# Kernel optimization log

Measured on AMD Instinct MI355X. Metric: run time of the kernel, lower is better.

Reference implementation:

```python
import jax, jax.numpy as jnp
import numpy as np

B, S, D_MODEL = 2, 2048, 2048
D_STATE, D_CONV, EXPAND = 16, 4, 2
D_INNER = EXPAND * D_MODEL  # 4096


def setup_inputs() -> dict:
    key = jax.random.key(0)
    ks = jax.random.split(key, 7)
    nrm = lambda k, shape, sc: jax.random.normal(k, shape, jnp.float32) * sc
    x = nrm(ks[0], (B, S, D_MODEL), 1.0)
    W_in = nrm(ks[1], (2 * D_INNER, D_MODEL), 0.02)          # in_proj (no bias)
    conv_w = nrm(ks[2], (D_INNER, 1, D_CONV), 0.1)            # depthwise conv1d
    conv_b = nrm(ks[3], (D_INNER,), 0.02)
    W_dt = nrm(ks[4], (D_INNER, D_INNER), 0.001)              # dt_proj weight
    b_dt = jnp.full((D_INNER,), -8.0, jnp.float32)            # keeps softplus(dt) tiny -> stable scan
    A_log = jnp.log(jnp.arange(1, D_STATE + 1, dtype=jnp.float32))[None, :]  # [1, d_state]
    W_out = nrm(ks[5], (D_MODEL, D_INNER), 1e-4)              # out_proj (no bias)
    return dict(x=x, W_in=W_in, conv_w=conv_w, conv_b=conv_b,
                W_dt=W_dt, b_dt=b_dt, A_log=A_log, W_out=W_out)


def reference(x, W_in, conv_w, conv_b, W_dt, b_dt, A_log, W_out):
    # in_proj then split into ssm branch and gate
    xz = jnp.einsum('bsd,ed->bse', x, W_in)            # [B,S,2*D_INNER]
    xi, gate = jnp.split(xz, 2, axis=-1)
    # depthwise causal conv (torch pads d_conv-1 both sides then truncates to S == left-pad only)
    xc = jnp.transpose(xi, (0, 2, 1))                  # [B,D_INNER,S]
    xc = jax.lax.conv_general_dilated(
        xc, conv_w, window_strides=(1,), padding=[(D_CONV - 1, 0)],
        dimension_numbers=('NCH', 'OIH', 'NCH'), feature_group_count=D_INNER)
    xc = xc + conv_b[None, :, None]
    xs = jax.nn.silu(jnp.transpose(xc, (0, 2, 1)))     # [B,S,D_INNER]
    # selective scan (only first d_state channels of x and dt are used)
    A = -jnp.exp(A_log[0])                             # [D_STATE]
    dt = jax.nn.softplus(jnp.einsum('bsd,ed->bse', xs, W_dt[:D_STATE]) + b_dt[:D_STATE])  # [B,S,D_STATE]
    u = xs[:, :, :D_STATE]                             # [B,S,D_STATE]

    def step(h, inp):
        x_t, dt_t = inp
        h = h * (1.0 + dt_t) + x_t
        return h, (h * A).sum(-1)                      # y_t: [B]

    h0 = jnp.zeros((B, D_STATE), xs.dtype)
    _, ys = jax.lax.scan(step, h0, (jnp.swapaxes(u, 0, 1), jnp.swapaxes(dt, 0, 1)))
    result = jnp.swapaxes(ys, 0, 1)                    # [B,S]
    # original: expand to d_inner, sum (== *d_inner), broadcast back over d_inner
    ssm_out = jnp.broadcast_to((result * D_INNER)[..., None], (B, S, D_INNER))
    y = ssm_out * jax.nn.sigmoid(gate)
    return jnp.einsum('bse,de->bsd', y, W_out)         # [B,S,D_MODEL]
```

## Files before the change

kernel.cpp:

```cpp
#include <hip/hip_runtime.h>
#include <hip/hip_bf16.h>
#include <math.h>

using bf16_t = __bf16;
using bf16x8 = __attribute__((ext_vector_type(8))) __bf16;
using f32x4  = __attribute__((ext_vector_type(4))) float;

typedef __attribute__((address_space(1))) const void* gas_ptr;
typedef __attribute__((address_space(3))) void*       las_ptr;

#define BATCH    2
#define SEQ      2048
#define DMODEL   2048
#define DINNER   4096
#define DSTATE   16
#define NROWS    (BATCH * SEQ)

#define CAST_C0  (2 * DINNER * DMODEL / 8)
#define CAST_C1  (NROWS * DMODEL / 8)
#define CAST_C2  (DMODEL * DINNER / 8)
#define CAST_BLOCKS ((CAST_C0 + CAST_C1 + CAST_C2) / 256)

__global__ __launch_bounds__(256)
void cast_all_kernel(const float* __restrict__ s0, bf16_t* __restrict__ d0,
                     const float* __restrict__ s1, bf16_t* __restrict__ d1,
                     const float* __restrict__ s2, bf16_t* __restrict__ d2)
{
    int i = blockIdx.x * 256 + threadIdx.x;
    const float* src; bf16_t* dst; int j;
    if (i < CAST_C0)                  { src = s0; dst = d0; j = i; }
    else if (i < CAST_C0 + CAST_C1)   { src = s1; dst = d1; j = i - CAST_C0; }
    else                              { src = s2; dst = d2; j = i - CAST_C0 - CAST_C1; }
    size_t off = (size_t)j * 8;
    float4 a = *(const float4*)(src + off);
    float4 b = *(const float4*)(src + off + 4);
    bf16x8 o;
    o[0] = (bf16_t)a.x; o[1] = (bf16_t)a.y; o[2] = (bf16_t)a.z; o[3] = (bf16_t)a.w;
    o[4] = (bf16_t)b.x; o[5] = (bf16_t)b.y; o[6] = (bf16_t)b.z; o[7] = (bf16_t)b.w;
    *(bf16x8*)(dst + off) = o;
}

#define GBAR()     asm volatile("s_barrier" ::: "memory")
#define WLGKM0()   asm volatile("s_waitcnt lgkmcnt(0)" ::: "memory")
#define WVM0()     asm volatile("s_waitcnt vmcnt(0)" ::: "memory")

#define MM(m, n, av, bv) \
    acc[m][n] = __builtin_amdgcn_mfma_f32_16x16x32_bf16(av, bv, acc[m][n], 0, 0, 0)

#define MFMA_COL2(nA, nB, bA, bB)                                   \
    MM(0, nA, a0, bA); MM(0, nB, a0, bB); MM(1, nA, a1, bA); MM(1, nB, a1, bB); \
    MM(2, nA, a2, bA); MM(2, nB, a2, bB); MM(3, nA, a3, bA); MM(3, nB, a3, bB); \
    MM(4, nA, a4, bA); MM(4, nB, a4, bB); MM(5, nA, a5, bA); MM(5, nB, a5, bB); \
    MM(6, nA, a6, bA); MM(6, nB, a6, bB); MM(7, nA, a7, bA); MM(7, nB, a7, bB)

__global__ __launch_bounds__(512, 2)
void gemm1_256(const bf16_t* __restrict__ A, const bf16_t* __restrict__ B,
               float* __restrict__ outf, bf16_t* __restrict__ outg)
{
    constexpr int K  = DMODEL;
    constexpr int NT = K / 64;

    __shared__ bf16_t As[2][256 * 64];
    __shared__ bf16_t Bs[2][256 * 64];

    const int t    = threadIdx.x;
    const int w    = t >> 6;
    const int lane = t & 63;
    const int wm   = w >> 2;
    const int wn   = w & 3;
    const int lo   = lane & 15;
    const int q    = lane >> 4;
    const int swz  = lo & 7;

    const int m0 = blockIdx.y * 256;
    const int n0 = blockIdx.x * 256;

    const int r_l   = lane >> 3;
    const int cb    = (lane & 7) ^ r_l;
    const int laneg = r_l * K + cb * 8;

    const bf16_t* Abase = A + (size_t)(m0 + w * 32) * K;
    const bf16_t* Bbase = B + (size_t)(n0 + w * 32) * K;

#define STAGE_A(BUF, kk) do {                                                  \
    _Pragma("unroll")                                                          \
    for (int c = 0; c < 4; ++c)                                                \
        __builtin_amdgcn_global_load_lds(                                      \
            (gas_ptr)(Abase + (kk) + c * 8 * K + laneg),                       \
            (las_ptr)&As[BUF][(w * 32 + c * 8) * 64], 16, 0, 0);               \
} while (0)
#define STAGE_B(BUF, kk) do {                                                  \
    _Pragma("unroll")                                                          \
    for (int c = 0; c < 4; ++c)                                                \
        __builtin_amdgcn_global_load_lds(                                      \
            (gas_ptr)(Bbase + (kk) + c * 8 * K + laneg),                       \
            (las_ptr)&Bs[BUF][(w * 32 + c * 8) * 64], 16, 0, 0);               \
} while (0)

#define LDA_F(BUF, m, s) \
    (*(const bf16x8*)&As[BUF][(wm * 128 + (m) * 16 + lo) * 64 + ((((s) * 4 + q) ^ swz) * 8)])
#define LDB_F(BUF, n, s) \
    (*(const bf16x8*)&Bs[BUF][(wn * 64  + (n) * 16 + lo) * 64 + ((((s) * 4 + q) ^ swz) * 8)])

    f32x4 acc[8][4];
#pragma unroll
    for (int i = 0; i < 8; ++i)
#pragma unroll
        for (int j = 0; j < 4; ++j) acc[i][j] = (f32x4){0.f, 0.f, 0.f, 0.f};

    STAGE_A(0, 0);
    STAGE_B(0, 0);
    WVM0();
    GBAR();

#define TILE_STEP(CUR, NXT, tkv) do {                                          \
    const int  k1_  = ((tkv) + 1) * 64;                                        \
    const bool pre_ = ((tkv) + 1) < NT;                                        \
    bf16x8 a0, a1, a2, a3, a4, a5, a6, a7, b0, b1, b2, b3;                     \
                   \
    a0 = LDA_F(CUR, 0, 0); a1 = LDA_F(CUR, 1, 0);                              \
    a2 = LDA_F(CUR, 2, 0); a3 = LDA_F(CUR, 3, 0);                              \
    a4 = LDA_F(CUR, 4, 0); a5 = LDA_F(CUR, 5, 0);                              \
    a6 = LDA_F(CUR, 6, 0); a7 = LDA_F(CUR, 7, 0);                              \
    b0 = LDB_F(CUR, 0, 0); b1 = LDB_F(CUR, 1, 0);                              \
    if (pre_) STAGE_A(NXT, k1_);                                               \
    GBAR(); WLGKM0();                                                          \
    __builtin_amdgcn_s_setprio(1);                                             \
    MFMA_COL2(0, 1, b0, b1);                                                   \
    __builtin_amdgcn_s_setprio(0);                                             \
    GBAR();                                                                    \
                                \
    b2 = LDB_F(CUR, 2, 0); b3 = LDB_F(CUR, 3, 0);                              \
    if (pre_) STAGE_B(NXT, k1_);                                               \
    GBAR(); WLGKM0();                                                          \
    __builtin_amdgcn_s_setprio(1);                                             \
    MFMA_COL2(2, 3, b2, b3);                                                   \
    __builtin_amdgcn_s_setprio(0);                                             \
    GBAR();                                                                    \
                                  \
    a0 = LDA_F(CUR, 0, 1); a1 = LDA_F(CUR, 1, 1);                              \
    a2 = LDA_F(CUR, 2, 1); a3 = LDA_F(CUR, 3, 1);                              \
    a4 = LDA_F(CUR, 4, 1); a5 = LDA_F(CUR, 5, 1);                              \
    a6 = LDA_F(CUR, 6, 1); a7 = LDA_F(CUR, 7, 1);                              \
    b0 = LDB_F(CUR, 0, 1); b1 = LDB_F(CUR, 1, 1);                              \
    GBAR(); WLGKM0();                                                          \
    __builtin_amdgcn_s_setprio(1);                                             \
    MFMA_COL2(0, 1, b0, b1);                                                   \
    __builtin_amdgcn_s_setprio(0);                                             \
    GBAR();                                                                    \
           \
    b2 = LDB_F(CUR, 2, 1); b3 = LDB_F(CUR, 3, 1);                              \
    GBAR(); WLGKM0();                                                          \
    __builtin_amdgcn_s_setprio(1);                                             \
    MFMA_COL2(2, 3, b2, b3);                                                   \
    __builtin_amdgcn_s_setprio(0);                                             \
    WVM0();                                                                    \
    GBAR();                                                                    \
} while (0)

#pragma unroll 1
    for (int tk = 0; tk < NT; tk += 2) {
        TILE_STEP(0, 1, tk);
        TILE_STEP(1, 0, tk + 1);
    }

#pragma unroll
    for (int m = 0; m < 8; ++m) {
        const int rbase = m0 + wm * 128 + m * 16 + q * 4;
#pragma unroll
        for (int n = 0; n < 4; ++n) {
            const int col = n0 + wn * 64 + n * 16 + lo;
#pragma unroll
            for (int rr = 0; rr < 4; ++rr) {
                float v   = acc[m][n][rr];
                int   row = rbase + rr;
                if (col < DINNER) {
                    outf[(size_t)row * DINNER + col] = v;
                } else {
                    float sg = 1.f / (1.f + __expf(-v));
                    outg[(size_t)row * DINNER + (col - DINNER)] = (bf16_t)sg;
                }
            }
        }
    }
}

__global__ __launch_bounds__(256)
void gemm_bt2(const bf16_t* __restrict__ A, const bf16_t* __restrict__ B, int K,
              float* __restrict__ outf, const float* __restrict__ rowscale)
{
    constexpr int LDK = 64;
    __shared__ bf16_t As[128 * LDK];
    __shared__ bf16_t Bs[128 * LDK];

    const int t    = threadIdx.x;
    const int m0   = blockIdx.y * 128;
    const int n0   = blockIdx.x * 128;
    const int w    = t >> 6;
    const int lane = t & 63;
    const int wr   = (w >> 1) * 64;
    const int wc   = (w & 1) * 64;
    const int lo   = lane & 15;
    const int q    = lane >> 4;

    const int r_l  = lane >> 3;
    const int cb   = (lane & 7) ^ r_l;
    const int laneA = (w * 32 + r_l) * K + cb * 8;
    const bf16_t* Abase = A + (size_t)m0 * K;
    const bf16_t* Bbase = B + (size_t)n0 * K;

    f32x4 acc[4][4];
#pragma unroll
    for (int i = 0; i < 4; ++i)
#pragma unroll
        for (int j = 0; j < 4; ++j) acc[i][j] = (f32x4){0.f, 0.f, 0.f, 0.f};

    for (int k0 = 0; k0 < K; k0 += 64) {
#pragma unroll
        for (int c = 0; c < 4; ++c) {
            const int uoff   = k0 + c * 8 * K;
            const int lo_off = (w * 32 + c * 8) * LDK;
            __builtin_amdgcn_global_load_lds((gas_ptr)(Abase + uoff + laneA),
                                             (las_ptr)&As[lo_off], 16, 0, 0);
            __builtin_amdgcn_global_load_lds((gas_ptr)(Bbase + uoff + laneA),
                                             (las_ptr)&Bs[lo_off], 16, 0, 0);
        }
        __syncthreads();

        const int swz = lo & 7;
#pragma unroll
        for (int ks = 0; ks < 2; ++ks) {
            const int kk = ((ks * 4 + q) ^ swz) * 8;
            bf16x8 af[4], bfv[4];
#pragma unroll
            for (int mi = 0; mi < 4; ++mi)
                af[mi] = *(const bf16x8*)&As[(wr + mi * 16 + lo) * LDK + kk];
#pragma unroll
            for (int ni = 0; ni < 4; ++ni)
                bfv[ni] = *(const bf16x8*)&Bs[(wc + ni * 16 + lo) * LDK + kk];
#pragma unroll
            for (int mi = 0; mi < 4; ++mi)
#pragma unroll
                for (int ni = 0; ni < 4; ++ni)
                    acc[mi][ni] = __builtin_amdgcn_mfma_f32_16x16x32_bf16(
                        af[mi], bfv[ni], acc[mi][ni], 0, 0, 0);
        }
        __syncthreads();
    }

#pragma unroll
    for (int mi = 0; mi < 4; ++mi) {
#pragma unroll
        for (int ni = 0; ni < 4; ++ni) {
            const int col   = n0 + wc + ni * 16 + lo;
            const int rbase = m0 + wr + mi * 16 + q * 4;
#pragma unroll
            for (int rr = 0; rr < 4; ++rr) {
                int row = rbase + rr;
                outf[(size_t)row * DMODEL + col] =
                    acc[mi][ni][rr] * (4096.0f * rowscale[row]);
            }
        }
    }
}

#define RROWS 4
__global__ __launch_bounds__(256)
void conv_dt_kernel(const float* __restrict__ xi, const float* __restrict__ cw,
                    const float* __restrict__ cbias, const float* __restrict__ wdt,
                    const float* __restrict__ bdt, float* __restrict__ uT,
                    float* __restrict__ dtT)
{
    const int r0 = blockIdx.x * RROWS;
    const int t  = threadIdx.x;
    const int s0 = r0 & (SEQ - 1);
    const int b  = r0 >> 11;

    float xsv[RROWS][16];
#pragma unroll
    for (int j = 0; j < 4; ++j) {
        const int c = t * 4 + j * 1024;
        float4 w0 = *(const float4*)(cw + (c + 0) * 4);
        float4 w1 = *(const float4*)(cw + (c + 1) * 4);
        float4 w2 = *(const float4*)(cw + (c + 2) * 4);
        float4 w3 = *(const float4*)(cw + (c + 3) * 4);
        float4 cbv = *(const float4*)(cbias + c);
        float4 xr[RROWS + 3];
#pragma unroll
        for (int i = 0; i < RROWS + 3; ++i) {
            int ss = s0 - 3 + i;
            if (ss >= 0)
                xr[i] = *(const float4*)(xi + (size_t)(r0 - 3 + i) * DINNER + c);
            else
                xr[i] = make_float4(0.f, 0.f, 0.f, 0.f);
        }
#pragma unroll
        for (int rr = 0; rr < RROWS; ++rr) {
            float4 a = xr[rr], bv = xr[rr + 1], cc = xr[rr + 2], d = xr[rr + 3];
            float v0 = cbv.x + w0.x * a.x + w0.y * bv.x + w0.z * cc.x + w0.w * d.x;
            float v1 = cbv.y + w1.x * a.y + w1.y * bv.y + w1.z * cc.y + w1.w * d.y;
            float v2 = cbv.z + w2.x * a.z + w2.y * bv.z + w2.z * cc.z + w2.w * d.z;
            float v3 = cbv.w + w3.x * a.w + w3.y * bv.w + w3.z * cc.w + w3.w * d.w;
            xsv[rr][j * 4 + 0] = v0 / (1.f + __expf(-v0));
            xsv[rr][j * 4 + 1] = v1 / (1.f + __expf(-v1));
            xsv[rr][j * 4 + 2] = v2 / (1.f + __expf(-v2));
            xsv[rr][j * 4 + 3] = v3 / (1.f + __expf(-v3));
        }
    }

    if (t < 4) {
#pragma unroll
        for (int rr = 0; rr < RROWS; ++rr)
#pragma unroll
            for (int k = 0; k < 4; ++k)
                uT[b * (DSTATE * SEQ) + (t * 4 + k) * SEQ + (s0 + rr)] = xsv[rr][k];
    }

    float acc[DSTATE][RROWS];
#pragma unroll
    for (int e = 0; e < DSTATE; ++e)
#pragma unroll
        for (int rr = 0; rr < RROWS; ++rr) acc[e][rr] = 0.f;

#pragma unroll
    for (int e = 0; e < DSTATE; ++e) {
        const float* wrow = wdt + (size_t)e * DINNER;
#pragma unroll
        for (int j = 0; j < 4; ++j) {
            float4 wv = *(const float4*)(wrow + t * 4 + j * 1024);
#pragma unroll
            for (int rr = 0; rr < RROWS; ++rr)
                acc[e][rr] += wv.x * xsv[rr][j * 4 + 0] + wv.y * xsv[rr][j * 4 + 1]
                            + wv.z * xsv[rr][j * 4 + 2] + wv.w * xsv[rr][j * 4 + 3];
        }
    }

#pragma unroll
    for (int e = 0; e < DSTATE; ++e)
#pragma unroll
        for (int rr = 0; rr < RROWS; ++rr) {
            float v = acc[e][rr];
#pragma unroll
            for (int off = 32; off > 0; off >>= 1) v += __shfl_down(v, off);
            acc[e][rr] = v;
        }
    __shared__ float red[4][DSTATE][RROWS];
    const int w = t >> 6;
    if ((t & 63) == 0) {
#pragma unroll
        for (int e = 0; e < DSTATE; ++e)
#pragma unroll
            for (int rr = 0; rr < RROWS; ++rr) red[w][e][rr] = acc[e][rr];
    }
    __syncthreads();
    if (t < 64) {
        int e = t >> 2, rr = t & 3;
        float tot = red[0][e][rr] + red[1][e][rr] + red[2][e][rr] + red[3][e][rr] + bdt[e];
        float dtv = (tot > 20.f) ? tot : log1pf(__expf(tot));
        dtT[b * (DSTATE * SEQ) + e * SEQ + (s0 + rr)] = dtv;
    }
}

__global__ __launch_bounds__(512)
void scan2_kernel(const float* __restrict__ dtT, const float* __restrict__ uT,
                  const float* __restrict__ A_log, float* __restrict__ result)
{
    __shared__ float cont[SEQ * 17];
    __shared__ float segP[DSTATE][32];
    __shared__ float segH[DSTATE][32];
    __shared__ float hin[DSTATE][32];

    const int b   = blockIdx.x;
    const int t   = threadIdx.x;
    const int n   = t >> 5;
    const int seg = t & 31;
    const float An = -expf(A_log[n]);

    const float* dtp = dtT + b * (DSTATE * SEQ) + n * SEQ + seg * 64;
    const float* up  = uT  + b * (DSTATE * SEQ) + n * SEQ + seg * 64;

    float P = 1.f, H = 0.f;
    for (int i = 0; i < 64; i += 4) {
        float4 dv = *(const float4*)(dtp + i);
        float4 uv = *(const float4*)(up + i);
        float a;
        a = 1.f + dv.x; P *= a; H = H * a + uv.x;
        a = 1.f + dv.y; P *= a; H = H * a + uv.y;
        a = 1.f + dv.z; P *= a; H = H * a + uv.z;
        a = 1.f + dv.w; P *= a; H = H * a + uv.w;
    }
    segP[n][seg] = P;
    segH[n][seg] = H;
    __syncthreads();

    if (t < DSTATE) {
        float h = 0.f;
#pragma unroll
        for (int j = 0; j < 32; ++j) {
            hin[t][j] = h;
            h = segP[t][j] * h + segH[t][j];
        }
    }
    __syncthreads();

    {
        float h = hin[n][seg];
        const int nsw = (n + seg) & 15;
        for (int i = 0; i < 64; i += 4) {
            float4 dv = *(const float4*)(dtp + i);
            float4 uv = *(const float4*)(up + i);
            const int s = seg * 64 + i;
            h = h * (1.f + dv.x) + uv.x; cont[(s + 0) * 17 + nsw] = h * An;
            h = h * (1.f + dv.y) + uv.y; cont[(s + 1) * 17 + nsw] = h * An;
            h = h * (1.f + dv.z) + uv.z; cont[(s + 2) * 17 + nsw] = h * An;
            h = h * (1.f + dv.w) + uv.w; cont[(s + 3) * 17 + nsw] = h * An;
        }
    }
    __syncthreads();

#pragma unroll
    for (int k = 0; k < 4; ++k) {
        const int s = t + k * 512;
        float sum = 0.f;
#pragma unroll
        for (int j = 0; j < DSTATE; ++j) sum += cont[s * 17 + j];
        result[b * SEQ + s] = sum;
    }
}

extern "C" void kernel_launch(void* const* d_in, const int* in_sizes, int n_in,
                              void* d_out, int out_size, void* d_ws, size_t ws_size,
                              hipStream_t stream)
{
    const float* x      = (const float*)d_in[0];
    const float* W_in   = (const float*)d_in[1];
    const float* conv_w = (const float*)d_in[2];
    const float* conv_b = (const float*)d_in[3];
    const float* W_dt   = (const float*)d_in[4];
    const float* b_dt   = (const float*)d_in[5];
    const float* A_log  = (const float*)d_in[6];
    const float* W_out  = (const float*)d_in[7];
    float* out = (float*)d_out;

    const size_t MB = 1u << 20;
    char* w = (char*)d_ws;
    bf16_t* xb   = (bf16_t*)(w);
    bf16_t* wib  = (bf16_t*)(w + 16 * MB);
    bf16_t* wob  = (bf16_t*)(w + 48 * MB);
    float*  xi   = (float*) (w + 64 * MB);
    bf16_t* g    = (bf16_t*)(w + 128 * MB);
    float*  uT   = (float*) (w + 160 * MB);
    float*  dtT  = (float*) (w + 160 * MB + 262144);
    float*  res  = (float*) (w + 160 * MB + 2 * 262144);

    cast_all_kernel<<<CAST_BLOCKS, 256, 0, stream>>>(W_in, wib, x, xb, W_out, wob);

    gemm1_256<<<dim3(32, 16), 512, 0, stream>>>(xb, wib, xi, g);

    conv_dt_kernel<<<NROWS / RROWS, 256, 0, stream>>>(xi, conv_w, conv_b, W_dt, b_dt, uT, dtT);

    scan2_kernel<<<2, 512, 0, stream>>>(dtT, uT, A_log, res);

    gemm_bt2<<<dim3(16, 32), 256, 0, stream>>>(g, wob, DINNER, out, res);
}
```

Before: 510.8 us.

## Split conv/dt kernel and compute dt projection with bf16 MFMA

Splits the fused conv+SiLU+dt-projection kernel in two. The first kernel writes SiLU outputs as bf16 to a workspace buffer. A new MFMA kernel computes the 16-wide dt projection from that buffer, using a bf16 copy of W_dt added to the cast kernel. This replaces the scalar FMA dot products, shuffle reductions and register pressure with matrix instructions. In exchange it adds an extra launch, a roughly 32MB bf16 write and read round trip, and bf16 precision on the dt inputs.

```diff
diff --git a/kernel.cpp b/kernel.cpp
--- a/kernel.cpp
+++ b/kernel.cpp
@@ -3,6 +3,7 @@
 #include <math.h>
 
 using bf16_t = __bf16;
+using bf16x4 = __attribute__((ext_vector_type(4))) __bf16;
 using bf16x8 = __attribute__((ext_vector_type(8))) __bf16;
 using f32x4  = __attribute__((ext_vector_type(4))) float;
 
@@ -19,18 +20,21 @@
 #define CAST_C0  (2 * DINNER * DMODEL / 8)
 #define CAST_C1  (NROWS * DMODEL / 8)
 #define CAST_C2  (DMODEL * DINNER / 8)
-#define CAST_BLOCKS ((CAST_C0 + CAST_C1 + CAST_C2) / 256)
+#define CAST_C3  (DSTATE * DINNER / 8)
+#define CAST_BLOCKS ((CAST_C0 + CAST_C1 + CAST_C2 + CAST_C3) / 256)
 
 __global__ __launch_bounds__(256)
 void cast_all_kernel(const float* __restrict__ s0, bf16_t* __restrict__ d0,
                      const float* __restrict__ s1, bf16_t* __restrict__ d1,
-                     const float* __restrict__ s2, bf16_t* __restrict__ d2)
+                     const float* __restrict__ s2, bf16_t* __restrict__ d2,
+                     const float* __restrict__ s3, bf16_t* __restrict__ d3)
 {
     int i = blockIdx.x * 256 + threadIdx.x;
     const float* src; bf16_t* dst; int j;
-    if (i < CAST_C0)                  { src = s0; dst = d0; j = i; }
-    else if (i < CAST_C0 + CAST_C1)   { src = s1; dst = d1; j = i - CAST_C0; }
-    else                              { src = s2; dst = d2; j = i - CAST_C0 - CAST_C1; }
+    if (i < CAST_C0)                            { src = s0; dst = d0; j = i; }
+    else if (i < CAST_C0 + CAST_C1)             { src = s1; dst = d1; j = i - CAST_C0; }
+    else if (i < CAST_C0 + CAST_C1 + CAST_C2)   { src = s2; dst = d2; j = i - CAST_C0 - CAST_C1; }
+    else                                        { src = s3; dst = d3; j = i - CAST_C0 - CAST_C1 - CAST_C2; }
     size_t off = (size_t)j * 8;
     float4 a = *(const float4*)(src + off);
     float4 b = *(const float4*)(src + off + 4);
@@ -266,17 +270,15 @@
 
 #define RROWS 4
 __global__ __launch_bounds__(256)
-void conv_dt_kernel(const float* __restrict__ xi, const float* __restrict__ cw,
-                    const float* __restrict__ cbias, const float* __restrict__ wdt,
-                    const float* __restrict__ bdt, float* __restrict__ uT,
-                    float* __restrict__ dtT)
+void conv_silu_kernel(const float* __restrict__ xi, const float* __restrict__ cw,
+                      const float* __restrict__ cbias,
+                      bf16_t* __restrict__ xs, float* __restrict__ uT)
 {
     const int r0 = blockIdx.x * RROWS;
     const int t  = threadIdx.x;
     const int s0 = r0 & (SEQ - 1);
     const int b  = r0 >> 11;
 
-    float xsv[RROWS][16];
 #pragma unroll
     for (int j = 0; j < 4; ++j) {
         const int c = t * 4 + j * 1024;
@@ -301,63 +303,58 @@
             float v1 = cbv.y + w1.x * a.y + w1.y * bv.y + w1.z * cc.y + w1.w * d.y;
             float v2 = cbv.z + w2.x * a.z + w2.y * bv.z + w2.z * cc.z + w2.w * d.z;
             float v3 = cbv.w + w3.x * a.w + w3.y * bv.w + w3.z * cc.w + w3.w * d.w;
-            xsv[rr][j * 4 + 0] = v0 / (1.f + __expf(-v0));
-            xsv[rr][j * 4 + 1] = v1 / (1.f + __expf(-v1));
-            xsv[rr][j * 4 + 2] = v2 / (1.f + __expf(-v2));
-            xsv[rr][j * 4 + 3] = v3 / (1.f + __expf(-v3));
-        }
-    }
-
-    if (t < 4) {
-#pragma unroll
-        for (int rr = 0; rr < RROWS; ++rr)
-#pragma unroll
-            for (int k = 0; k < 4; ++k)
-                uT[b * (DSTATE * SEQ) + (t * 4 + k) * SEQ + (s0 + rr)] = xsv[rr][k];
-    }
-
-    float acc[DSTATE][RROWS];
-#pragma unroll
-    for (int e = 0; e < DSTATE; ++e)
-#pragma unroll
-        for (int rr = 0; rr < RROWS; ++rr) acc[e][rr] = 0.f;
-
-#pragma unroll
-    for (int e = 0; e < DSTATE; ++e) {
-        const float* wrow = wdt + (size_t)e * DINNER;
-#pragma unroll
-        for (int j = 0; j < 4; ++j) {
-            float4 wv = *(const float4*)(wrow + t * 4 + j * 1024);
-#pragma unroll
-            for (int rr = 0; rr < RROWS; ++rr)
-                acc[e][rr] += wv.x * xsv[rr][j * 4 + 0] + wv.y * xsv[rr][j * 4 + 1]
-                            + wv.z * xsv[rr][j * 4 + 2] + wv.w * xsv[rr][j * 4 + 3];
-        }
-    }
-
-#pragma unroll
-    for (int e = 0; e < DSTATE; ++e)
-#pragma unroll
-        for (int rr = 0; rr < RROWS; ++rr) {
-            float v = acc[e][rr];
-#pragma unroll
-            for (int off = 32; off > 0; off >>= 1) v += __shfl_down(v, off);
-            acc[e][rr] = v;
-        }
-    __shared__ float red[4][DSTATE][RROWS];
-    const int w = t >> 6;
-    if ((t & 63) == 0) {
-#pragma unroll
-        for (int e = 0; e < DSTATE; ++e)
-#pragma unroll
-            for (int rr = 0; rr < RROWS; ++rr) red[w][e][rr] = acc[e][rr];
-    }
+            float o0 = v0 / (1.f + __expf(-v0));
+            float o1 = v1 / (1.f + __expf(-v1));
+            float o2 = v2 / (1.f + __expf(-v2));
+            float o3 = v3 / (1.f + __expf(-v3));
+            bf16x4 ov;
+            ov[0] = (bf16_t)o0; ov[1] = (bf16_t)o1;
+            ov[2] = (bf16_t)o2; ov[3] = (bf16_t)o3;
+            *(bf16x4*)(xs + (size_t)(r0 + rr) * DINNER + c) = ov;
+            if (j == 0 && t < 4) {
+                uT[b * (DSTATE * SEQ) + (c + 0) * SEQ + (s0 + rr)] = o0;
+                uT[b * (DSTATE * SEQ) + (c + 1) * SEQ + (s0 + rr)] = o1;
+                uT[b * (DSTATE * SEQ) + (c + 2) * SEQ + (s0 + rr)] = o2;
+                uT[b * (DSTATE * SEQ) + (c + 3) * SEQ + (s0 + rr)] = o3;
+            }
+        }
+    }
+}
+
+__global__ __launch_bounds__(256)
+void dt_mfma_kernel(const bf16_t* __restrict__ xs, const bf16_t* __restrict__ wdtb,
+                    const float* __restrict__ bdt, float* __restrict__ dtT)
+{
+    __shared__ float red[4][256];
+    const int t    = threadIdx.x;
+    const int w    = t >> 6;
+    const int lane = t & 63;
+    const int lo   = lane & 15;
+    const int q    = lane >> 4;
+    const int r0   = blockIdx.x * 16;
+
+    const bf16_t* arow = xs   + (size_t)(r0 + lo) * DINNER + w * 1024 + q * 8;
+    const bf16_t* brow = wdtb + (size_t)lo        * DINNER + w * 1024 + q * 8;
+
+    f32x4 acc = (f32x4){0.f, 0.f, 0.f, 0.f};
+#pragma unroll
+    for (int kt = 0; kt < 32; ++kt) {
+        bf16x8 a  = *(const bf16x8*)(arow + kt * 32);
+        bf16x8 bv = *(const bf16x8*)(brow + kt * 32);
+        acc = __builtin_amdgcn_mfma_f32_16x16x32_bf16(a, bv, acc, 0, 0, 0);
+    }
+#pragma unroll
+    for (int i = 0; i < 4; ++i) red[w][lane * 4 + i] = acc[i];
     __syncthreads();
-    if (t < 64) {
-        int e = t >> 2, rr = t & 3;
-        float tot = red[0][e][rr] + red[1][e][rr] + red[2][e][rr] + red[3][e][rr] + bdt[e];
-        float dtv = (tot > 20.f) ? tot : log1pf(__expf(tot));
-        dtT[b * (DSTATE * SEQ) + e * SEQ + (s0 + rr)] = dtv;
+
+    {
+        const int ln  = t >> 2;
+        const int i   = t & 3;
+        const int e   = ln & 15;
+        const int row = r0 + (ln >> 4) * 4 + i;
+        float v = red[0][t] + red[1][t] + red[2][t] + red[3][t] + bdt[e];
+        float dtv = (v > 20.f) ? v : log1pf(__expf(v));
+        dtT[(row >> 11) * (DSTATE * SEQ) + e * SEQ + (row & (SEQ - 1))] = dtv;
     }
 }
 
@@ -452,12 +449,17 @@
     float*  uT   = (float*) (w + 160 * MB);
     float*  dtT  = (float*) (w + 160 * MB + 262144);
     float*  res  = (float*) (w + 160 * MB + 2 * 262144);
-
-    cast_all_kernel<<<CAST_BLOCKS, 256, 0, stream>>>(W_in, wib, x, xb, W_out, wob);
+    bf16_t* xs   = (bf16_t*)(w + 161 * MB);
+    bf16_t* wdtb = (bf16_t*)(w + 193 * MB);
+
+    cast_all_kernel<<<CAST_BLOCKS, 256, 0, stream>>>(W_in, wib, x, xb, W_out, wob,
+                                                     W_dt, wdtb);
 
     gemm1_256<<<dim3(32, 16), 512, 0, stream>>>(xb, wib, xi, g);
 
-    conv_dt_kernel<<<NROWS / RROWS, 256, 0, stream>>>(xi, conv_w, conv_b, W_dt, b_dt, uT, dtT);
+    conv_silu_kernel<<<NROWS / RROWS, 256, 0, stream>>>(xi, conv_w, conv_b, xs, uT);
+
+    dt_mfma_kernel<<<NROWS / 16, 256, 0, stream>>>(xs, wdtb, b_dt, dtT);
 
     scan2_kernel<<<2, 512, 0, stream>>>(dtT, uT, A_log, res);
 
```

Measured after the change: 465.8 us. 1.1x faster.
